# Kernel optimization log

Measured on AMD Instinct MI355X. Metric: run time of the kernel, lower is better.

## Reference

```python
import jax, jax.numpy as jnp
import numpy as np

L = 2048
E = 1024
H = 16
D = E // H


def setup_inputs() -> dict:
    key = jax.random.key(0)
    ks = jax.random.split(key, 9)
    inp = {
        "values": jax.random.normal(ks[0], (L, E), dtype=jnp.float32),
        "keys": jax.random.normal(ks[1], (L, E), dtype=jnp.float32),
        "query": jax.random.normal(ks[2], (L, E), dtype=jnp.float32),
        "dist_matrix": jax.random.uniform(ks[3], (L, L), dtype=jnp.float32),
        "Wv": jax.random.normal(ks[4], (E, E), dtype=jnp.float32) * 0.02,
        "Wk": jax.random.normal(ks[5], (E, E), dtype=jnp.float32) * 0.02,
        "Wq": jax.random.normal(ks[6], (E, E), dtype=jnp.float32) * 0.02,
        "Wo": jax.random.normal(ks[7], (E, E), dtype=jnp.float32) * 0.02,
        "bo": jax.random.normal(ks[8], (E,), dtype=jnp.float32) * 0.02,
    }
    return inp


def reference(values, keys, query, dist_matrix, Wv, Wk, Wq, Wo, bo):
    # Linear projections (torch Linear: x @ W.T), then split heads: [L, H, D]
    v = (values @ Wv.T).reshape(L, H, D)
    k = (keys @ Wk.T).reshape(L, H, D)
    q = (query @ Wq.T).reshape(L, H, D)

    # energy: [H, Lq, Lk]
    energy = jnp.einsum("qhd,khd->hqk", q, k)

    # distance bias: zeros -> inf, then 1/(d+1); broadcast over heads
    dm = jnp.where(dist_matrix == 0, jnp.inf, dist_matrix)
    bias = 1.0 / (dm + 1.0)
    energy = energy + bias[None, :, :]

    attn = jax.nn.softmax(energy / jnp.sqrt(jnp.float32(E)), axis=2)

    out = jnp.einsum("hql,lhd->qhd", attn, v).reshape(L, H * D)
    return out @ Wo.T + bo
```

## Files before the change

kernel.cpp:

```cpp
#include <hip/hip_runtime.h>


#define L_SEQ 2048
#define E_DIM 1024
#define H_HEADS 16
#define D_HEAD 64
#define KSPLIT 4

typedef unsigned short u16;
typedef unsigned int u32;
typedef __attribute__((ext_vector_type(8))) short bf16x8;
typedef __attribute__((ext_vector_type(8))) unsigned short u16x8;
typedef __attribute__((ext_vector_type(4))) unsigned short u16x4;
typedef __attribute__((ext_vector_type(4))) float f32x4;

#define C_LOG2E_32 0.045084220027780106f

__device__ __forceinline__ float bf2f(u16 u) {
  union { u32 i; float f; } v; v.i = ((u32)u) << 16; return v.f;
}
__device__ __forceinline__ u16 f2bf(float f) {
  union { float f; u32 i; } v; v.f = f;
  u32 u = v.i;
  u += 0x7FFFu + ((u >> 16) & 1u);
  return (u16)(u >> 16);
}
__device__ __forceinline__ u32 pack_bf16_pair(float lo, float hi) {
  union { float f; u32 u; } a, b;
  a.f = lo; b.f = hi;
  return __builtin_amdgcn_perm(b.u + 0x8000u, a.u + 0x8000u, 0x07060302u);
}
__device__ __forceinline__ void gload16(const u16* g, u16* l) {
  __builtin_amdgcn_global_load_lds(
      (const __attribute__((address_space(1))) u32*)g,
      (__attribute__((address_space(3))) u32*)l, 16, 0, 0);
}

__global__ void cvt_all(const float* __restrict__ xq, const float* __restrict__ xk,
                        const float* __restrict__ xv,
                        const float* __restrict__ wq, const float* __restrict__ wk,
                        const float* __restrict__ wv, const float* __restrict__ wo,
                        const float* __restrict__ dist,
                        u16* oq, u16* ok, u16* ov,
                        u16* owq, u16* owk, u16* owv, u16* owo, u16* obias)
{
  size_t gid = (size_t)blockIdx.x * 256 + threadIdx.x;
  const size_t NQ = 524288;
  const size_t NW = 262144;
  const float* src; u16* dst; size_t off; bool isb = false;
  if      (gid <     NQ)           { src = xq;   dst = oq;    off = gid; }
  else if (gid < 2 * NQ)           { src = xk;   dst = ok;    off = gid - NQ; }
  else if (gid < 3 * NQ)           { src = xv;   dst = ov;    off = gid - 2 * NQ; }
  else if (gid < 3 * NQ + NW)      { src = wq;   dst = owq;   off = gid - 3 * NQ; }
  else if (gid < 3 * NQ + 2 * NW)  { src = wk;   dst = owk;   off = gid - 3 * NQ - NW; }
  else if (gid < 3 * NQ + 3 * NW)  { src = wv;   dst = owv;   off = gid - 3 * NQ - 2 * NW; }
  else if (gid < 3 * NQ + 4 * NW)  { src = wo;   dst = owo;   off = gid - 3 * NQ - 3 * NW; }
  else { src = dist; dst = obias; off = gid - 3 * NQ - 4 * NW; isb = true; }

  f32x4 v = *(const f32x4*)&src[off * 4];
  u16x4 o;
#pragma unroll
  for (int j = 0; j < 4; ++j) {
    float f = v[j];
    if (isb) f = (f == 0.f) ? 0.f : C_LOG2E_32 / (f + 1.f);
    o[j] = f2bf(f);
  }
  *(u16x4*)&dst[off * 4] = o;
}

#define TM 128
#define TN 128
#define BK 32

template<int OUTMODE>
__global__ __launch_bounds__(256, 2) void gemm_bt3b(
    const u16* __restrict__ A0, const u16* __restrict__ B0, void* __restrict__ C0,
    const u16* __restrict__ A1, const u16* __restrict__ B1, void* __restrict__ C1,
    const u16* __restrict__ A2, const u16* __restrict__ B2, void* __restrict__ C2,
    const float* __restrict__ bias, int M, int N, int K)
{
  const u16* A; const u16* B; void* C;
  if (blockIdx.z == 0)      { A = A0; B = B0; C = C0; }
  else if (blockIdx.z == 1) { A = A1; B = B1; C = C1; }
  else                      { A = A2; B = B2; C = C2; }

  __shared__ __align__(16) u16 As[TM][BK];
  __shared__ __align__(16) u16 Bs[TN][BK];

  const int m0 = blockIdx.y * TM;
  const int n0 = blockIdx.x * TN;
  const int t = threadIdx.x;
  const int wave = t >> 6;
  const int lane = t & 63;
  const int quad = lane >> 4;
  const int col  = lane & 15;
  const int wm = (wave >> 1) * 64;
  const int wn = (wave & 1) * 64;

  const int lr = lane >> 2;
  const int lc = (lane & 3) * 8;
  const u16* gA = A + (size_t)(m0 + wave * 32 + lr) * K + lc;
  const u16* gB = B + (size_t)(n0 + wave * 32 + lr) * K + lc;
  u16* lA0 = &As[wave * 32][0];
  u16* lA1 = &As[wave * 32 + 16][0];
  u16* lB0 = &Bs[wave * 32][0];
  u16* lB1 = &Bs[wave * 32 + 16][0];

  f32x4 acc[4][4];
#pragma unroll
  for (int i = 0; i < 4; ++i)
#pragma unroll
    for (int j = 0; j < 4; ++j) acc[i][j] = (f32x4){0.f, 0.f, 0.f, 0.f};

  for (int k0 = 0; k0 < K; k0 += BK) {
    __syncthreads();
    gload16(gA + k0, lA0);
    gload16(gA + (size_t)16 * K + k0, lA1);
    gload16(gB + k0, lB0);
    gload16(gB + (size_t)16 * K + k0, lB1);
    __syncthreads();

    bf16x8 af[4], bfr[4];
#pragma unroll
    for (int i = 0; i < 4; ++i)
      af[i] = *(const bf16x8*)&As[wm + i * 16 + col][quad * 8];
#pragma unroll
    for (int j = 0; j < 4; ++j)
      bfr[j] = *(const bf16x8*)&Bs[wn + j * 16 + col][quad * 8];

#pragma unroll
    for (int i = 0; i < 4; ++i)
#pragma unroll
      for (int j = 0; j < 4; ++j)
        acc[i][j] = __builtin_amdgcn_mfma_f32_16x16x32_bf16(af[i], bfr[j], acc[i][j], 0, 0, 0);
  }

  const bool transC = (OUTMODE == 0) && (blockIdx.z == 2);
#pragma unroll
  for (int i = 0; i < 4; ++i) {
    int rowb = m0 + wm + i * 16 + quad * 4;
#pragma unroll
    for (int j = 0; j < 4; ++j) {
      int cn = n0 + wn + j * 16 + col;
      if (OUTMODE == 1) {
        float badd = bias ? bias[cn] : 0.f;
#pragma unroll
        for (int r = 0; r < 4; ++r)
          ((float*)C)[(size_t)(rowb + r) * N + cn] = acc[i][j][r] + badd;
      } else if (transC) {
        u16x4 pk;
#pragma unroll
        for (int r = 0; r < 4; ++r) pk[r] = f2bf(acc[i][j][r]);
        *(u16x4*)&((u16*)C)[(size_t)cn * M + rowb] = pk;
      } else {
#pragma unroll
        for (int r = 0; r < 4; ++r)
          ((u16*)C)[(size_t)(rowb + r) * N + cn] = f2bf(acc[i][j][r]);
      }
    }
  }
}

#define FK 64
#define LDV 72

__global__ __launch_bounds__(256, 5) void flash3(
    const u16* __restrict__ Q, const u16* __restrict__ Kp,
    const u16* __restrict__ Vt, const u16* __restrict__ Bb,
    u16* __restrict__ Op, float* __restrict__ lp)
{
  __shared__ __align__(16) u16 Ks[FK][LDV];
  __shared__ __align__(16) u16 Vs[D_HEAD][LDV];
  __shared__ __align__(16) u16 Ps[4][16][LDV];

  const int h  = blockIdx.y;
  const int q0 = blockIdx.x * 64;
  const int z  = blockIdx.z;
  const int hoff = h * D_HEAD;
  const int kbase = z * (L_SEQ / KSPLIT);
  const int t = threadIdx.x;
  const int wave = t >> 6;
  const int lane = t & 63;
  const int quad = lane >> 4;
  const int col  = lane & 15;

  bf16x8 qf[2];
  {
    const u16* qrow = Q + (size_t)(q0 + wave * 16 + col) * E_DIM + hoff;
    qf[0] = *(const bf16x8*)(qrow + quad * 8);
    qf[1] = *(const bf16x8*)(qrow + 32 + quad * 8);
  }

  float l_lane = 0.f;
  f32x4 oacc[4];
#pragma unroll
  for (int td = 0; td < 4; ++td) oacc[td] = (f32x4){0.f, 0.f, 0.f, 0.f};

  const u16* brow = Bb + (size_t)(q0 + wave * 16 + col) * L_SEQ;
  const int cst = t & 7, rst = t >> 3;

  for (int kt = 0; kt < L_SEQ / KSPLIT / FK; ++kt) {
    const int k0 = kbase + kt * FK;
    __syncthreads();
#pragma unroll
    for (int s = 0; s < 2; ++s) {
      int rr = rst + s * 32;
      *(u16x8*)&Ks[rr][cst * 8] = *(const u16x8*)&Kp[(size_t)(k0 + rr) * E_DIM + hoff + cst * 8];
      *(u16x8*)&Vs[rr][cst * 8] = *(const u16x8*)&Vt[(size_t)(hoff + rr) * L_SEQ + k0 + cst * 8];
    }
    float pb[4][4];
#pragma unroll
    for (int tt = 0; tt < 4; ++tt) {
      u16x4 bv = *(const u16x4*)&brow[k0 + tt * 16 + quad * 4];
#pragma unroll
      for (int r = 0; r < 4; ++r) pb[tt][r] = bf2f(bv[r]);
    }
    __syncthreads();

#pragma unroll
    for (int tt = 0; tt < 4; ++tt) {
      f32x4 a = (f32x4){0.f, 0.f, 0.f, 0.f};
      a = __builtin_amdgcn_mfma_f32_16x16x32_bf16(*(const bf16x8*)&Ks[tt * 16 + col][quad * 8], qf[0], a, 0, 0, 0);
      a = __builtin_amdgcn_mfma_f32_16x16x32_bf16(*(const bf16x8*)&Ks[tt * 16 + col][32 + quad * 8], qf[1], a, 0, 0, 0);
      float p[4];
#pragma unroll
      for (int r = 0; r < 4; ++r) {
        p[r] = __builtin_amdgcn_exp2f(fmaf(a[r], C_LOG2E_32, pb[tt][r]));
        l_lane += p[r];
      }
      uint2 w;
      w.x = pack_bf16_pair(p[0], p[1]);
      w.y = pack_bf16_pair(p[2], p[3]);
      *(uint2*)&Ps[wave][col][tt * 16 + quad * 4] = w;
    }

#pragma unroll
    for (int kk = 0; kk < 2; ++kk) {
      bf16x8 pf = *(const bf16x8*)&Ps[wave][col][kk * 32 + quad * 8];
#pragma unroll
      for (int td = 0; td < 4; ++td) {
        bf16x8 vf = *(const bf16x8*)&Vs[td * 16 + col][kk * 32 + quad * 8];
        oacc[td] = __builtin_amdgcn_mfma_f32_16x16x32_bf16(pf, vf, oacc[td], 0, 0, 0);
      }
    }
  }

  l_lane += __shfl_xor(l_lane, 16);
  l_lane += __shfl_xor(l_lane, 32);
  if (lane < 16)
    lp[((size_t)z * L_SEQ + q0 + wave * 16 + lane) * H_HEADS + h] = l_lane;

  const int qrow_mine = q0 + wave * 16 + quad * 4;
#pragma unroll
  for (int td = 0; td < 4; ++td)
#pragma unroll
    for (int r = 0; r < 4; ++r)
      Op[((size_t)z * L_SEQ + qrow_mine + r) * E_DIM + hoff + td * 16 + col] = f2bf(oacc[td][r]);
}

__global__ void merge_attn(const u16* __restrict__ Op, const float* __restrict__ lp,
                           u16* __restrict__ AOb)
{
  size_t gid = (size_t)blockIdx.x * 256 + threadIdx.x;
  size_t idx = gid * 4;
  int q = (int)(idx >> 10);
  int e = (int)(idx & 1023);
  int h = e >> 6;
  float o[4] = {0.f, 0.f, 0.f, 0.f};
  float lsum = 0.f;
#pragma unroll
  for (int s = 0; s < KSPLIT; ++s) {
    u16x4 pv = *(const u16x4*)&Op[((size_t)s * L_SEQ + q) * E_DIM + e];
#pragma unroll
    for (int j = 0; j < 4; ++j) o[j] += bf2f(pv[j]);
    lsum += lp[((size_t)s * L_SEQ + q) * H_HEADS + h];
  }
  float inv = 1.f / lsum;
  u16x4 pk;
#pragma unroll
  for (int j = 0; j < 4; ++j) pk[j] = f2bf(o[j] * inv);
  *(u16x4*)&AOb[idx] = pk;
}

extern "C" void kernel_launch(void* const* d_in, const int* in_sizes, int n_in,
                              void* d_out, int out_size, void* d_ws, size_t ws_size,
                              hipStream_t stream)
{
  const float* values = (const float*)d_in[0];
  const float* keys   = (const float*)d_in[1];
  const float* query  = (const float*)d_in[2];
  const float* dist   = (const float*)d_in[3];
  const float* Wv     = (const float*)d_in[4];
  const float* Wk     = (const float*)d_in[5];
  const float* Wq     = (const float*)d_in[6];
  const float* Wo     = (const float*)d_in[7];
  const float* bo     = (const float*)d_in[8];
  float* out = (float*)d_out;

  const size_t MB = (size_t)1 << 20;
  char* w = (char*)d_ws;
  u16* xq  = (u16*)(w + 0 * MB);
  u16* xk  = (u16*)(w + 4 * MB);
  u16* xv  = (u16*)(w + 8 * MB);
  u16* wqb = (u16*)(w + 12 * MB);
  u16* wkb = (u16*)(w + 14 * MB);
  u16* wvb = (u16*)(w + 16 * MB);
  u16* wob = (u16*)(w + 18 * MB);
  u16* Bb  = (u16*)(w + 20 * MB);
  u16* Qh  = (u16*)(w + 28 * MB);
  u16* Kh  = (u16*)(w + 32 * MB);
  u16* Vth = (u16*)(w + 36 * MB);
  u16* AOb = (u16*)(w + 40 * MB);
  float* lp = (float*)(w + 44 * MB);
  u16* Op  = (u16*)(w + 0 * MB);

  cvt_all<<<14336, 256, 0, stream>>>(query, keys, values, Wq, Wk, Wv, Wo, dist,
                                     xq, xk, xv, wqb, wkb, wvb, wob, Bb);

  dim3 gProj(E_DIM / TN, L_SEQ / TM, 3);
  gemm_bt3b<0><<<gProj, 256, 0, stream>>>(xq, wqb, Qh,
                                          xk, wkb, Kh,
                                          xv, wvb, Vth,
                                          nullptr, L_SEQ, E_DIM, E_DIM);

  dim3 gAttn(L_SEQ / 64, H_HEADS, KSPLIT);
  flash3<<<gAttn, 256, 0, stream>>>(Qh, Kh, Vth, Bb, Op, lp);

  merge_attn<<<(L_SEQ * E_DIM / 4) / 256, 256, 0, stream>>>(Op, lp, AOb);

  dim3 gOut(E_DIM / TN, L_SEQ / TM, 1);
  gemm_bt3b<1><<<gOut, 256, 0, stream>>>(AOb, wob, out,
                                         AOb, wob, out,
                                         AOb, wob, out,
                                         bo, L_SEQ, E_DIM, E_DIM);
}
```

Baseline: 218.2 us.

## Widen GEMM K-tile with XOR-swizzled LDS and split-K output projection via atomics

```diff
diff --git a/kernel.cpp b/kernel.cpp
--- a/kernel.cpp
+++ b/kernel.cpp
@@ -68,24 +68,32 @@
   *(u16x4*)&dst[off * 4] = o;
 }
 
+__global__ void bias_fill(const float* __restrict__ bo, float* __restrict__ out)
+{
+  size_t gid = (size_t)blockIdx.x * 256 + threadIdx.x;
+  int n = (int)((gid * 4) & (E_DIM - 1));
+  *(f32x4*)&out[gid * 4] = *(const f32x4*)&bo[n];
+}
+
 #define TM 128
 #define TN 128
-#define BK 32
+#define BK 64
 
 template<int OUTMODE>
-__global__ __launch_bounds__(256, 2) void gemm_bt3b(
+__global__ __launch_bounds__(256, 2) void gemm_bt3c(
     const u16* __restrict__ A0, const u16* __restrict__ B0, void* __restrict__ C0,
     const u16* __restrict__ A1, const u16* __restrict__ B1, void* __restrict__ C1,
     const u16* __restrict__ A2, const u16* __restrict__ B2, void* __restrict__ C2,
-    const float* __restrict__ bias, int M, int N, int K)
+    int M, int N, int K)
 {
   const u16* A; const u16* B; void* C;
-  if (blockIdx.z == 0)      { A = A0; B = B0; C = C0; }
+  if (OUTMODE == 2)         { A = A0; B = B0; C = C0; }
+  else if (blockIdx.z == 0) { A = A0; B = B0; C = C0; }
   else if (blockIdx.z == 1) { A = A1; B = B1; C = C1; }
   else                      { A = A2; B = B2; C = C2; }
 
-  __shared__ __align__(16) u16 As[TM][BK];
-  __shared__ __align__(16) u16 Bs[TN][BK];
+  __shared__ __align__(16) u16 As[TM * BK];
+  __shared__ __align__(16) u16 Bs[TN * BK];
 
   const int m0 = blockIdx.y * TM;
   const int n0 = blockIdx.x * TN;
@@ -97,14 +105,13 @@
   const int wm = (wave >> 1) * 64;
   const int wn = (wave & 1) * 64;
 
-  const int lr = lane >> 2;
-  const int lc = (lane & 3) * 8;
-  const u16* gA = A + (size_t)(m0 + wave * 32 + lr) * K + lc;
-  const u16* gB = B + (size_t)(n0 + wave * 32 + lr) * K + lc;
-  u16* lA0 = &As[wave * 32][0];
-  u16* lA1 = &As[wave * 32 + 16][0];
-  u16* lB0 = &Bs[wave * 32][0];
-  u16* lB1 = &Bs[wave * 32 + 16][0];
+  const int roff = lane >> 3;
+  const int gcol = ((lane & 7) ^ roff) * 8;
+  const u16* gA = A + (size_t)(m0 + wave * 32 + roff) * K + gcol;
+  const u16* gB = B + (size_t)(n0 + wave * 32 + roff) * K + gcol;
+
+  const int kbeg = (OUTMODE == 2) ? blockIdx.z * (K / KSPLIT) : 0;
+  const int kend = (OUTMODE == 2) ? kbeg + K / KSPLIT : K;
 
   f32x4 acc[4][4];
 #pragma unroll
@@ -112,27 +119,36 @@
 #pragma unroll
     for (int j = 0; j < 4; ++j) acc[i][j] = (f32x4){0.f, 0.f, 0.f, 0.f};
 
-  for (int k0 = 0; k0 < K; k0 += BK) {
+  const int c7 = col & 7;
+
+  for (int k0 = kbeg; k0 < kend; k0 += BK) {
     __syncthreads();
-    gload16(gA + k0, lA0);
-    gload16(gA + (size_t)16 * K + k0, lA1);
-    gload16(gB + k0, lB0);
-    gload16(gB + (size_t)16 * K + k0, lB1);
+#pragma unroll
+    for (int s = 0; s < 4; ++s) {
+      gload16(gA + (size_t)(s * 8) * K + k0, &As[(wave * 32 + s * 8) * BK]);
+      gload16(gB + (size_t)(s * 8) * K + k0, &Bs[(wave * 32 + s * 8) * BK]);
+    }
     __syncthreads();
 
-    bf16x8 af[4], bfr[4];
-#pragma unroll
-    for (int i = 0; i < 4; ++i)
-      af[i] = *(const bf16x8*)&As[wm + i * 16 + col][quad * 8];
-#pragma unroll
-    for (int j = 0; j < 4; ++j)
-      bfr[j] = *(const bf16x8*)&Bs[wn + j * 16 + col][quad * 8];
-
-#pragma unroll
-    for (int i = 0; i < 4; ++i)
+    bf16x8 af[4][2], bfr[4][2];
+#pragma unroll
+    for (int ks = 0; ks < 2; ++ks) {
+      const int slot = ((ks * 4 + quad) ^ c7) * 8;
+#pragma unroll
+      for (int i = 0; i < 4; ++i)
+        af[i][ks] = *(const bf16x8*)&As[(wm + i * 16 + col) * BK + slot];
 #pragma unroll
       for (int j = 0; j < 4; ++j)
-        acc[i][j] = __builtin_amdgcn_mfma_f32_16x16x32_bf16(af[i], bfr[j], acc[i][j], 0, 0, 0);
+        bfr[j][ks] = *(const bf16x8*)&Bs[(wn + j * 16 + col) * BK + slot];
+    }
+
+#pragma unroll
+    for (int ks = 0; ks < 2; ++ks)
+#pragma unroll
+      for (int i = 0; i < 4; ++i)
+#pragma unroll
+        for (int j = 0; j < 4; ++j)
+          acc[i][j] = __builtin_amdgcn_mfma_f32_16x16x32_bf16(af[i][ks], bfr[j][ks], acc[i][j], 0, 0, 0);
   }
 
   const bool transC = (OUTMODE == 0) && (blockIdx.z == 2);
@@ -142,11 +158,10 @@
 #pragma unroll
     for (int j = 0; j < 4; ++j) {
       int cn = n0 + wn + j * 16 + col;
-      if (OUTMODE == 1) {
-        float badd = bias ? bias[cn] : 0.f;
+      if (OUTMODE == 2) {
 #pragma unroll
         for (int r = 0; r < 4; ++r)
-          ((float*)C)[(size_t)(rowb + r) * N + cn] = acc[i][j][r] + badd;
+          unsafeAtomicAdd(&((float*)C)[(size_t)(rowb + r) * N + cn], acc[i][j][r]);
       } else if (transC) {
         u16x4 pk;
 #pragma unroll
@@ -317,20 +332,22 @@
   cvt_all<<<14336, 256, 0, stream>>>(query, keys, values, Wq, Wk, Wv, Wo, dist,
                                      xq, xk, xv, wqb, wkb, wvb, wob, Bb);
 
+  bias_fill<<<(L_SEQ * E_DIM / 4) / 256, 256, 0, stream>>>(bo, out);
+
   dim3 gProj(E_DIM / TN, L_SEQ / TM, 3);
-  gemm_bt3b<0><<<gProj, 256, 0, stream>>>(xq, wqb, Qh,
+  gemm_bt3c<0><<<gProj, 256, 0, stream>>>(xq, wqb, Qh,
                                           xk, wkb, Kh,
                                           xv, wvb, Vth,
-                                          nullptr, L_SEQ, E_DIM, E_DIM);
+                                          L_SEQ, E_DIM, E_DIM);
 
   dim3 gAttn(L_SEQ / 64, H_HEADS, KSPLIT);
   flash3<<<gAttn, 256, 0, stream>>>(Qh, Kh, Vth, Bb, Op, lp);
 
   merge_attn<<<(L_SEQ * E_DIM / 4) / 256, 256, 0, stream>>>(Op, lp, AOb);
 
-  dim3 gOut(E_DIM / TN, L_SEQ / TM, 1);
-  gemm_bt3b<1><<<gOut, 256, 0, stream>>>(AOb, wob, out,
+  dim3 gOut(E_DIM / TN, L_SEQ / TM, KSPLIT);
+  gemm_bt3c<2><<<gOut, 256, 0, stream>>>(AOb, wob, out,
                                          AOb, wob, out,
                                          AOb, wob, out,
-                                         bo, L_SEQ, E_DIM, E_DIM);
-}
+                                         L_SEQ, E_DIM, E_DIM);
+}
```

Result: slower. 223.0 us (+2.2%).
